# Optimization experiments

Hardware: AMD Instinct MI355X
Metric: run time of the kernel (lower is better)

Reference implementation:

```python
import jax, jax.numpy as jnp
import numpy as np
import math

B, T, C, D = 8, 2048, 1024, 1024
N_LAYER, LAYER_ID = 24, 12


def setup_inputs() -> dict:
    key = jax.random.key(0)
    ks = jax.random.split(key, 5)
    r01 = LAYER_ID / (N_LAYER - 1)
    r10 = 1.0 - LAYER_ID / N_LAYER
    ddd = np.arange(C, dtype=np.float64) / C                      # (C,)
    h = np.arange(D, dtype=np.float64)
    decay_speed = -5 + 8 * (h / (D - 1)) ** (0.7 + 1.3 * r01)     # time_decay init
    zigzag = ((np.arange(D) + 1) % 3 - 1) * 0.5
    time_first = np.log(0.3) + zigzag
    scale = C ** -0.5
    return {
        "x": jax.random.normal(ks[0], (B, T, C), jnp.float32),
        "time_decay": jnp.asarray(decay_speed, jnp.float32),
        "time_first": jnp.asarray(time_first, jnp.float32),
        "time_mix_k": jnp.asarray(ddd ** r10, jnp.float32),
        "time_mix_v": jnp.asarray(ddd ** r10 + 0.3 * r01, jnp.float32),
        "time_mix_r": jnp.asarray(ddd ** (0.5 * r10), jnp.float32),
        "Wk": jax.random.normal(ks[1], (D, C), jnp.float32) * scale,
        "Wv": jax.random.normal(ks[2], (D, C), jnp.float32) * scale,
        "Wr": jax.random.normal(ks[3], (D, C), jnp.float32) * scale,
        "Wo": jax.random.normal(ks[4], (C, D), jnp.float32) * scale,
    }


def _wkv(time_decay, time_first, k, v):
    # wkv_t = (e^{u+k_t} v_t + A_{t-1}) / (e^{u+k_t} + B_{t-1})
    # A_t = e^w A_{t-1} + e^{k_t} v_t ;  B_t likewise with v=1 ;  w = -exp(time_decay)
    # Exactly the math of the original conv1d-with-exp-curve trick, in O(T).
    ew = jnp.exp(-jnp.exp(time_decay))   # (D,)
    eu = jnp.exp(time_first)             # (D,)
    ek = jnp.exp(k)                      # [B,T,D]
    ekv = ek * v

    def step(carry, inp):
        a, b = carry                     # [B,D] each
        ekt, ekvt = inp                  # [B,D] each
        out = (eu * ekvt + a) / (eu * ekt + b)
        return (ew * a + ekvt, ew * b + ekt), out

    init = (jnp.zeros_like(ek[:, 0]), jnp.zeros_like(ek[:, 0]))
    xs = (jnp.swapaxes(ek, 0, 1), jnp.swapaxes(ekv, 0, 1))  # [T,B,D]
    _, out = jax.lax.scan(step, init, xs)
    return jnp.swapaxes(out, 0, 1)       # [B,T,D]


def reference(x, time_decay, time_first, time_mix_k, time_mix_v, time_mix_r, Wk, Wv, Wr, Wo):
    # time_shift: prepend zero row, drop last (ZeroPad2d((0,0,1,-1)))
    xx = jnp.pad(x, ((0, 0), (1, 0), (0, 0)))[:, :-1]
    xk = x * time_mix_k + xx * (1 - time_mix_k)
    xv = x * time_mix_v + xx * (1 - time_mix_v)
    xr = x * time_mix_r + xx * (1 - time_mix_r)
    k = jnp.einsum('btc,dc->btd', xk, Wk)
    v = jnp.einsum('btc,dc->btd', xv, Wv)
    sr = jax.nn.sigmoid(jnp.einsum('btc,dc->btd', xr, Wr))
    rwkv = sr * _wkv(time_decay, time_first, k, v)
    return jnp.einsum('btd,cd->btc', rwkv, Wo)
```

## Files before the change

kernel.cpp:

```cpp
#include <hip/hip_runtime.h>
#include <cstdint>
#include <cstddef>

#define Bb 8
#define Tt 2048
#define Cc 1024
#define Dd 1024
#define Mm (Bb*Tt)
#define CL 64
#define NCH (Tt/CL)


typedef __bf16  bf16x8  __attribute__((ext_vector_type(8)));
typedef float   floatx4 __attribute__((ext_vector_type(4)));

#define MFMA16(a, b, c) __builtin_amdgcn_mfma_f32_16x16x32_bf16((a), (b), (c), 0, 0, 0)

__device__ __forceinline__ ushort f2bf(float f) {
    unsigned u = __float_as_uint(f);
    u = (u + 0x7FFF + ((u >> 16) & 1)) >> 16;
    return (ushort)u;
}
__device__ __forceinline__ float bf2f(ushort u) {
    return __uint_as_float(((unsigned)u) << 16);
}

__device__ __forceinline__ void load_lds16(const void* g, void* l) {
    __builtin_amdgcn_global_load_lds((__attribute__((address_space(1))) void*)(g),
                                     (__attribute__((address_space(3))) void*)(l),
                                     16, 0, 0);
}

#define CFENCE asm volatile("" ::: "memory")
#define BARRIER do { CFENCE; __builtin_amdgcn_s_barrier(); CFENCE; } while (0)

__global__ __launch_bounds__(256) void prep_mix3(
        const float* __restrict__ x,
        const float* __restrict__ mk, const float* __restrict__ mv,
        const float* __restrict__ mr,
        ushort* __restrict__ xk, ushort* __restrict__ xv, ushort* __restrict__ xr) {
    int i  = blockIdx.x * 256 + threadIdx.x;
    int cq = i & (Cc / 8 - 1);
    int m  = i >> 7;
    int t  = m & (Tt - 1);
    float xc[8], xp[8];
    *(float4*)&xc[0] = ((const float4*)x)[i * 2];
    *(float4*)&xc[4] = ((const float4*)x)[i * 2 + 1];
    if (t != 0) {
        *(float4*)&xp[0] = ((const float4*)x)[(i - Cc / 8) * 2];
        *(float4*)&xp[4] = ((const float4*)x)[(i - Cc / 8) * 2 + 1];
    } else {
#pragma unroll
        for (int j = 0; j < 8; j++) xp[j] = 0.f;
    }
    float wk[8], wv[8], wr[8];
    *(float4*)&wk[0] = ((const float4*)mk)[cq * 2];
    *(float4*)&wk[4] = ((const float4*)mk)[cq * 2 + 1];
    *(float4*)&wv[0] = ((const float4*)mv)[cq * 2];
    *(float4*)&wv[4] = ((const float4*)mv)[cq * 2 + 1];
    *(float4*)&wr[0] = ((const float4*)mr)[cq * 2];
    *(float4*)&wr[4] = ((const float4*)mr)[cq * 2 + 1];
    ushort ok[8], ov[8], orr[8];
#pragma unroll
    for (int j = 0; j < 8; j++) {
        float d = xc[j] - xp[j];
        ok[j]  = f2bf(xp[j] + d * wk[j]);
        ov[j]  = f2bf(xp[j] + d * wv[j]);
        orr[j] = f2bf(xp[j] + d * wr[j]);
    }
    ((ulonglong2*)xk)[i] = *(const ulonglong2*)ok;
    ((ulonglong2*)xv)[i] = *(const ulonglong2*)ov;
    ((ulonglong2*)xr)[i] = *(const ulonglong2*)orr;
}

__global__ __launch_bounds__(256) void cvt_w(
        const float* __restrict__ wk, const float* __restrict__ wv,
        const float* __restrict__ wr, const float* __restrict__ wo,
        ushort* __restrict__ ok, ushort* __restrict__ ov,
        ushort* __restrict__ orr, ushort* __restrict__ oo) {
    int i = blockIdx.x * 256 + threadIdx.x;
    int sel = i >> 18;
    int j = i & ((1 << 18) - 1);
    const float* s = sel == 0 ? wk : sel == 1 ? wv : sel == 2 ? wr : wo;
    ushort* d      = sel == 0 ? ok : sel == 1 ? ov : sel == 2 ? orr : oo;
    float4 f = ((const float4*)s)[j];
    ushort4 o;
    o.x = f2bf(f.x); o.y = f2bf(f.y); o.z = f2bf(f.z); o.w = f2bf(f.w);
    ((ushort4*)d)[j] = o;
}

struct GemmR10 {
    floatx4 acc[8][4];
    int quad, fr, wm, wn;

    __device__ __forceinline__ void run(
            const ushort* __restrict__ A, const ushort* __restrict__ Bw,
            long tm, long tn, int Kdim, __bf16* LDSb) {
        const int tid  = threadIdx.x;
        const int lane = tid & 63;
        quad = lane >> 4;
        fr   = lane & 15;
        const int wave = tid >> 6;
        wm = (wave >> 2) * 128;
        wn = (wave & 3) * 64;
        const int goff = (quad ^ ((fr >> 1) & 3)) * 8;

        const int srow = tid >> 2;
        const int scol = ((tid & 3) ^ ((tid >> 3) & 3)) * 8;
        const int wlds = wave * 512;
        const ushort* Ag0 = A  + (tm + srow) * (long)Kdim + scol;
        const ushort* Ag1 = Ag0 + 128 * (long)Kdim;
        const ushort* Bg0 = Bw + (tn + srow) * (long)Kdim + scol;
        const ushort* Bg1 = Bg0 + 128 * (long)Kdim;

        auto stageA = [&](int buf, long ko) {
            __bf16* d = LDSb + buf * 16384;
            load_lds16(Ag0 + ko, d + wlds);
            load_lds16(Ag1 + ko, d + 4096 + wlds);
        };
        auto stageB = [&](int buf, long ko) {
            __bf16* d = LDSb + buf * 16384 + 8192;
            load_lds16(Bg0 + ko, d + wlds);
            load_lds16(Bg1 + ko, d + 4096 + wlds);
        };

        floatx4 zero = {0.f, 0.f, 0.f, 0.f};
#pragma unroll
        for (int ai = 0; ai < 8; ai++)
#pragma unroll
            for (int nj = 0; nj < 4; nj++) acc[ai][nj] = zero;

        const int NT = Kdim >> 5;

        stageA(0, 0);  stageB(0, 0);
        stageA(1, 32); stageB(1, 32);
        asm volatile("s_waitcnt vmcnt(4)" ::: "memory");
        BARRIER;

        int bc = 0;
        for (int T = 0; T < NT; ++T) {
            const __bf16* Ab = LDSb + bc * 16384;
            const __bf16* Bbf = Ab + 8192;
            const int sb = (bc + 2 >= 3) ? bc - 1 : bc + 2;
            const bool pf = (T + 2 < NT);
            const long ko = (long)(T + 2) * 32;

            bf16x8 a[8], b0, b1, b2, b3;
#pragma unroll
            for (int i = 0; i < 8; i++)
                a[i] = *(const bf16x8*)&Ab[(wm + i * 16 + fr) * 32 + goff];
            b0 = *(const bf16x8*)&Bbf[(wn + fr) * 32 + goff];
            b1 = *(const bf16x8*)&Bbf[(wn + 16 + fr) * 32 + goff];
            if (pf) stageA(sb, ko);
            BARRIER;
            __builtin_amdgcn_s_setprio(1);
#pragma unroll
            for (int i = 0; i < 8; i++) {
                acc[i][0] = MFMA16(a[i], b0, acc[i][0]);
                acc[i][1] = MFMA16(a[i], b1, acc[i][1]);
            }
            __builtin_amdgcn_s_setprio(0);
            BARRIER;

            b2 = *(const bf16x8*)&Bbf[(wn + 32 + fr) * 32 + goff];
            b3 = *(const bf16x8*)&Bbf[(wn + 48 + fr) * 32 + goff];
            if (pf) stageB(sb, ko);
            if (T + 1 < NT) {
                if (pf) asm volatile("s_waitcnt vmcnt(4)" ::: "memory");
                else    asm volatile("s_waitcnt vmcnt(0)" ::: "memory");
            }
            BARRIER;
            __builtin_amdgcn_s_setprio(1);
#pragma unroll
            for (int i = 0; i < 8; i++) {
                acc[i][2] = MFMA16(a[i], b2, acc[i][2]);
                acc[i][3] = MFMA16(a[i], b3, acc[i][3]);
            }
            __builtin_amdgcn_s_setprio(0);
            BARRIER;

            bc = (bc + 1 == 3) ? 0 : bc + 1;
        }
    }
};

template<int MODE>
__global__ __launch_bounds__(512, 2) void gemm_nt(
        const ushort* __restrict__ A, const ushort* __restrict__ Bw,
        void* __restrict__ Co, int Ndim, int Kdim) {
    __shared__ __attribute__((aligned(16))) __bf16 LDSb[3 * 16384];
    const int orig = blockIdx.y * 64 + blockIdx.x;
    const int L    = (orig & 7) * 32 + (orig >> 3);
    const long tm = (long)(L >> 2) * 256;
    const long tn = (long)(L & 3) * 256;
    GemmR10 g;
    g.run(A, Bw, tm, tn, Kdim, LDSb);
#pragma unroll
    for (int ai = 0; ai < 8; ai++)
#pragma unroll
        for (int nj = 0; nj < 4; nj++)
#pragma unroll
            for (int r = 0; r < 4; r++) {
                long grow = tm + g.wm + ai * 16 + g.quad * 4 + r;
                long gcol = tn + g.wn + nj * 16 + g.fr;
                float v = g.acc[ai][nj][r];
                if (MODE == 2) v = 1.f / (1.f + __expf(-v));
                if (MODE == 0)      ((float*)Co)[grow * Ndim + gcol] = v;
                else if (MODE == 3) ((_Float16*)Co)[grow * Ndim + gcol] = (_Float16)v;
                else                ((ushort*)Co)[grow * Ndim + gcol] = f2bf(v);
            }
}

__global__ __launch_bounds__(512, 2) void gemm3_nt(
        const ushort* __restrict__ xk, const ushort* __restrict__ xv,
        const ushort* __restrict__ xr,
        const ushort* __restrict__ wk, const ushort* __restrict__ wv,
        const ushort* __restrict__ wr,
        _Float16* __restrict__ kb, ushort* __restrict__ vb,
        ushort* __restrict__ sb) {
    __shared__ __attribute__((aligned(16))) __bf16 LDSb[3 * 16384];
    const int orig = blockIdx.y * 64 + blockIdx.x;
    const int L    = (orig & 7) * 96 + (orig >> 3);
    const int proj = L >> 8;
    const int rem  = L & 255;
    const long tm = (long)(rem >> 2) * 256;
    const long tn = (long)(rem & 3) * 256;
    const ushort* A  = proj == 0 ? xk : proj == 1 ? xv : xr;
    const ushort* Bw = proj == 0 ? wk : proj == 1 ? wv : wr;
    GemmR10 g;
    g.run(A, Bw, tm, tn, Cc, LDSb);
#pragma unroll
    for (int ai = 0; ai < 8; ai++)
#pragma unroll
        for (int nj = 0; nj < 4; nj++)
#pragma unroll
            for (int r = 0; r < 4; r++) {
                long grow = tm + g.wm + ai * 16 + g.quad * 4 + r;
                long gcol = tn + g.wn + nj * 16 + g.fr;
                long off = grow * Dd + gcol;
                float v = g.acc[ai][nj][r];
                if (proj == 0)      kb[off] = (_Float16)v;
                else if (proj == 1) vb[off] = f2bf(v);
                else                sb[off] = f2bf(1.f / (1.f + __expf(-v)));
            }
}

__global__ __launch_bounds__(256) void wkv_part(
        const _Float16* __restrict__ kb, const ushort* __restrict__ vb,
        const float* __restrict__ decay,
        float* __restrict__ pa, float* __restrict__ pb) {
    int gid = blockIdx.x * 256 + threadIdx.x;
    int d = gid & (Dd - 1);
    int c = (gid >> 10) & (NCH - 1);
    int b = gid >> 15;
    float ew = __expf(-__expf(decay[d]));
    size_t base = ((size_t)b * Tt + (size_t)c * CL) * Dd + d;
    float a = 0.f, bs = 0.f;
    for (int i0 = 0; i0 < CL; i0 += 8) {
        float kr[8], vr[8];
#pragma unroll
        for (int j = 0; j < 8; j++) {
            size_t idx = base + (size_t)(i0 + j) * Dd;
            kr[j] = (float)kb[idx]; vr[j] = bf2f(vb[idx]);
        }
#pragma unroll
        for (int j = 0; j < 8; j++) {
            float ek = __expf(kr[j]);
            a  = ew * a  + ek * vr[j];
            bs = ew * bs + ek;
        }
    }
    int sidx = c * (Bb * Dd) + b * Dd + d;
    pa[sidx] = a; pb[sidx] = bs;
}

__global__ __launch_bounds__(256) void wkv_prefix(
        const float* __restrict__ pa, const float* __restrict__ pb,
        const float* __restrict__ decay,
        float* __restrict__ sa, float* __restrict__ sb) {
    int gid = blockIdx.x * 256 + threadIdx.x;
    int d = gid & (Dd - 1);
    float ewL = __expf(-__expf(decay[d]) * (float)CL);
    float ca = 0.f, cb = 0.f;
#pragma unroll
    for (int c = 0; c < NCH; c++) {
        int idx = c * (Bb * Dd) + gid;
        sa[idx] = ca; sb[idx] = cb;
        ca = ewL * ca + pa[idx];
        cb = ewL * cb + pb[idx];
    }
}

__global__ __launch_bounds__(256) void wkv_chunk(
        const _Float16* __restrict__ kb, const ushort* __restrict__ vb,
        const ushort* __restrict__ sr,
        const float* __restrict__ decay, const float* __restrict__ tf,
        const float* __restrict__ sa, const float* __restrict__ sb,
        ushort* __restrict__ rw) {
    int gid = blockIdx.x * 256 + threadIdx.x;
    int d = gid & (Dd - 1);
    int c = (gid >> 10) & (NCH - 1);
    int b = gid >> 15;
    float ew = __expf(-__expf(decay[d]));
    float eu = __expf(tf[d]);
    int sidx = c * (Bb * Dd) + b * Dd + d;
    float a = sa[sidx], bs = sb[sidx];
    size_t base = ((size_t)b * Tt + (size_t)c * CL) * Dd + d;
    for (int i0 = 0; i0 < CL; i0 += 8) {
        float kr[8], vr[8], rr[8];
#pragma unroll
        for (int j = 0; j < 8; j++) {
            size_t idx = base + (size_t)(i0 + j) * Dd;
            kr[j] = (float)kb[idx]; vr[j] = bf2f(vb[idx]); rr[j] = bf2f(sr[idx]);
        }
#pragma unroll
        for (int j = 0; j < 8; j++) {
            float ek  = __expf(kr[j]);
            float ekv = ek * vr[j];
            float out = (eu * ekv + a) / (eu * ek + bs);
            a  = ew * a  + ekv;
            bs = ew * bs + ek;
            rw[base + (size_t)(i0 + j) * Dd] = f2bf(rr[j] * out);
        }
    }
}

extern "C" void kernel_launch(void* const* d_in, const int* in_sizes, int n_in,
                              void* d_out, int out_size, void* d_ws, size_t ws_size,
                              hipStream_t stream) {
    (void)in_sizes; (void)n_in; (void)out_size;
    const float* x  = (const float*)d_in[0];
    const float* td = (const float*)d_in[1];
    const float* tf = (const float*)d_in[2];
    const float* mk = (const float*)d_in[3];
    const float* mv = (const float*)d_in[4];
    const float* mr = (const float*)d_in[5];
    const float* Wk = (const float*)d_in[6];
    const float* Wv = (const float*)d_in[7];
    const float* Wr = (const float*)d_in[8];
    const float* Wo = (const float*)d_in[9];
    float* out = (float*)d_out;

    const size_t xsz = (size_t)Mm * Cc * 2;
    const size_t wsz = (size_t)Dd * Cc * 2;
    const size_t ssz = (size_t)Bb * NCH * Dd * 4;
    const size_t need_merged = 6 * xsz + 4 * wsz + 4 * ssz;

    char* p = (char*)d_ws;
    auto take = [&](size_t n) { char* r = p; p += n; return r; };
    ushort*   xk = (ushort*)take(xsz);
    ushort*   xv = (ushort*)take(xsz);
    ushort*   xr = (ushort*)take(xsz);
    _Float16* kb = (_Float16*)take(xsz);
    const bool merged = ws_size >= need_merged;
    ushort *vb, *sb, *rw;
    if (merged) {
        vb = (ushort*)take(xsz);
        sb = (ushort*)take(xsz);
        rw = xk;
    } else {
        vb = xk;
        sb = xv;
        rw = xr;
    }
    ushort* wk = (ushort*)take(wsz);
    ushort* wv = (ushort*)take(wsz);
    ushort* wr = (ushort*)take(wsz);
    ushort* wo = (ushort*)take(wsz);
    float*  pa = (float*)take(ssz);
    float*  pb = (float*)take(ssz);
    float*  sa = (float*)take(ssz);
    float*  sbst = (float*)take(ssz);

    dim3 g1(Mm / 256, Dd / 256);
    dim3 g2(Mm / 256, Cc / 256);
    dim3 g3(Mm / 256, 3 * Dd / 256);
    const int wkv_grid = (Bb * NCH * Dd) / 256;

    cvt_w<<<4096, 256, 0, stream>>>(Wk, Wv, Wr, Wo, wk, wv, wr, wo);
    prep_mix3<<<Mm * Cc / 8 / 256, 256, 0, stream>>>(x, mk, mv, mr, xk, xv, xr);

    if (merged) {
        gemm3_nt<<<g3, 512, 0, stream>>>(xk, xv, xr, wk, wv, wr, kb, vb, sb);
    } else {
        gemm_nt<3><<<g1, 512, 0, stream>>>(xk, wk, kb, Dd, Cc);
        gemm_nt<1><<<g1, 512, 0, stream>>>(xv, wv, vb, Dd, Cc);
        gemm_nt<2><<<g1, 512, 0, stream>>>(xr, wr, sb, Dd, Cc);
    }

    wkv_part  <<<wkv_grid, 256, 0, stream>>>(kb, vb, td, pa, pb);
    wkv_prefix<<<(Bb * Dd) / 256, 256, 0, stream>>>(pa, pb, td, sa, sbst);
    wkv_chunk <<<wkv_grid, 256, 0, stream>>>(kb, vb, sb, td, tf, sa, sbst, rw);

    gemm_nt<0><<<g2, 512, 0, stream>>>(rw, wo, out, Cc, Dd);
}
```

Measured before the change: 376.0 us.

## Pre-swizzle weights into MFMA fragment layout and load B directly to registers

The weight conversion kernel now writes bf16 weights in a fragment-packed layout, so the GEMM loads B operands straight from global memory into registers, double-buffered across K steps. Only A still goes through LDS, which halves LDS use and removes the B staging and one barrier pair per iteration. The WKV part and chunk kernels are also vectorised to handle 4 channels per thread with wider loads. The trade-off is that B fragments come from global/L2 without LDS reuse across waves, and fewer threads are available to hide scan latency.

```diff
diff --git a/kernel.cpp b/kernel.cpp
--- a/kernel.cpp
+++ b/kernel.cpp
@@ -13,6 +13,8 @@
 
 typedef __bf16  bf16x8  __attribute__((ext_vector_type(8)));
 typedef float   floatx4 __attribute__((ext_vector_type(4)));
+typedef _Float16 halfx4 __attribute__((ext_vector_type(4)));
+typedef unsigned short ushortx4 __attribute__((ext_vector_type(4)));
 
 #define MFMA16(a, b, c) __builtin_amdgcn_mfma_f32_16x16x32_bf16((a), (b), (c), 0, 0, 0)
 
@@ -79,22 +81,28 @@
         ushort* __restrict__ ok, ushort* __restrict__ ov,
         ushort* __restrict__ orr, ushort* __restrict__ oo) {
     int i = blockIdx.x * 256 + threadIdx.x;
-    int sel = i >> 18;
-    int j = i & ((1 << 18) - 1);
+    int fr  = i & 15;
+    int c8  = (i >> 4) & 127;
+    int nhi = (i >> 11) & 63;
+    int sel = i >> 17;
     const float* s = sel == 0 ? wk : sel == 1 ? wv : sel == 2 ? wr : wo;
     ushort* d      = sel == 0 ? ok : sel == 1 ? ov : sel == 2 ? orr : oo;
-    float4 f = ((const float4*)s)[j];
-    ushort4 o;
-    o.x = f2bf(f.x); o.y = f2bf(f.y); o.z = f2bf(f.z); o.w = f2bf(f.w);
-    ((ushort4*)d)[j] = o;
-}
-
-struct GemmR10 {
+    int n = nhi * 16 + fr;
+    const float4* src = (const float4*)(s + (size_t)n * Cc + c8 * 8);
+    float4 f0 = src[0], f1 = src[1];
+    ushort o[8];
+    o[0] = f2bf(f0.x); o[1] = f2bf(f0.y); o[2] = f2bf(f0.z); o[3] = f2bf(f0.w);
+    o[4] = f2bf(f1.x); o[5] = f2bf(f1.y); o[6] = f2bf(f1.z); o[7] = f2bf(f1.w);
+    int idx = (nhi * 32 + (c8 >> 2)) * 64 + (c8 & 3) * 16 + fr;
+    ((ulonglong2*)d)[idx] = *(const ulonglong2*)o;
+}
+
+struct GemmR11 {
     floatx4 acc[8][4];
     int quad, fr, wm, wn;
 
     __device__ __forceinline__ void run(
-            const ushort* __restrict__ A, const ushort* __restrict__ Bw,
+            const ushort* __restrict__ A, const ushort* __restrict__ Bp,
             long tm, long tn, int Kdim, __bf16* LDSb) {
         const int tid  = threadIdx.x;
         const int lane = tid & 63;
@@ -104,25 +112,21 @@
         wm = (wave >> 2) * 128;
         wn = (wave & 3) * 64;
         const int goff = (quad ^ ((fr >> 1) & 3)) * 8;
+        const int NKT  = Kdim >> 5;
 
         const int srow = tid >> 2;
         const int scol = ((tid & 3) ^ ((tid >> 3) & 3)) * 8;
         const int wlds = wave * 512;
-        const ushort* Ag0 = A  + (tm + srow) * (long)Kdim + scol;
+        const ushort* Ag0 = A + (tm + srow) * (long)Kdim + scol;
         const ushort* Ag1 = Ag0 + 128 * (long)Kdim;
-        const ushort* Bg0 = Bw + (tn + srow) * (long)Kdim + scol;
-        const ushort* Bg1 = Bg0 + 128 * (long)Kdim;
 
         auto stageA = [&](int buf, long ko) {
-            __bf16* d = LDSb + buf * 16384;
+            __bf16* d = LDSb + buf * 8192;
             load_lds16(Ag0 + ko, d + wlds);
             load_lds16(Ag1 + ko, d + 4096 + wlds);
         };
-        auto stageB = [&](int buf, long ko) {
-            __bf16* d = LDSb + buf * 16384 + 8192;
-            load_lds16(Bg0 + ko, d + wlds);
-            load_lds16(Bg1 + ko, d + 4096 + wlds);
-        };
+
+        const ushort* Bq = Bp + ((long)((tn + wn) >> 4)) * NKT * 512 + lane * 8;
 
         floatx4 zero = {0.f, 0.f, 0.f, 0.f};
 #pragma unroll
@@ -130,57 +134,57 @@
 #pragma unroll
             for (int nj = 0; nj < 4; nj++) acc[ai][nj] = zero;
 
-        const int NT = Kdim >> 5;
-
-        stageA(0, 0);  stageB(0, 0);
-        stageA(1, 32); stageB(1, 32);
-        asm volatile("s_waitcnt vmcnt(4)" ::: "memory");
+        const int NT = NKT;
+
+        stageA(0, 0);
+        stageA(1, 32);
+        bf16x8 bA[4], bB[4];
+#pragma unroll
+        for (int ni = 0; ni < 4; ni++)
+            bA[ni] = *(const bf16x8*)(Bq + (long)ni * NKT * 512);
+        asm volatile("s_waitcnt vmcnt(6)" ::: "memory");
         BARRIER;
 
-        int bc = 0;
-        for (int T = 0; T < NT; ++T) {
-            const __bf16* Ab = LDSb + bc * 16384;
-            const __bf16* Bbf = Ab + 8192;
-            const int sb = (bc + 2 >= 3) ? bc - 1 : bc + 2;
-            const bool pf = (T + 2 < NT);
-            const long ko = (long)(T + 2) * 32;
-
-            bf16x8 a[8], b0, b1, b2, b3;
-#pragma unroll
-            for (int i = 0; i < 8; i++)
-                a[i] = *(const bf16x8*)&Ab[(wm + i * 16 + fr) * 32 + goff];
-            b0 = *(const bf16x8*)&Bbf[(wn + fr) * 32 + goff];
-            b1 = *(const bf16x8*)&Bbf[(wn + 16 + fr) * 32 + goff];
-            if (pf) stageA(sb, ko);
-            BARRIER;
-            __builtin_amdgcn_s_setprio(1);
-#pragma unroll
-            for (int i = 0; i < 8; i++) {
-                acc[i][0] = MFMA16(a[i], b0, acc[i][0]);
-                acc[i][1] = MFMA16(a[i], b1, acc[i][1]);
-            }
-            __builtin_amdgcn_s_setprio(0);
-            BARRIER;
-
-            b2 = *(const bf16x8*)&Bbf[(wn + 32 + fr) * 32 + goff];
-            b3 = *(const bf16x8*)&Bbf[(wn + 48 + fr) * 32 + goff];
-            if (pf) stageB(sb, ko);
-            if (T + 1 < NT) {
-                if (pf) asm volatile("s_waitcnt vmcnt(4)" ::: "memory");
-                else    asm volatile("s_waitcnt vmcnt(0)" ::: "memory");
-            }
-            BARRIER;
-            __builtin_amdgcn_s_setprio(1);
-#pragma unroll
-            for (int i = 0; i < 8; i++) {
-                acc[i][2] = MFMA16(a[i], b2, acc[i][2]);
-                acc[i][3] = MFMA16(a[i], b3, acc[i][3]);
-            }
-            __builtin_amdgcn_s_setprio(0);
-            BARRIER;
-
-            bc = (bc + 1 == 3) ? 0 : bc + 1;
+        int slot = 0, snext = 2;
+
+#define R11_BODY(T, BC, BN)                                                   \
+        {                                                                     \
+            const __bf16* Ab = LDSb + slot * 8192;                            \
+            const bool pfB = (T) + 1 < NT;                                    \
+            const bool pfA = (T) + 2 < NT;                                    \
+            if (pfB) {                                                        \
+                _Pragma("unroll")                                             \
+                for (int ni = 0; ni < 4; ni++)                                \
+                    BN[ni] = *(const bf16x8*)(Bq + ((long)ni * NKT + (T) + 1) * 512); \
+            }                                                                 \
+            if (pfA) stageA(snext, (long)((T) + 2) * 32);                     \
+            bf16x8 a_[8];                                                     \
+            _Pragma("unroll")                                                 \
+            for (int i = 0; i < 8; i++)                                       \
+                a_[i] = *(const bf16x8*)&Ab[(wm + i * 16 + fr) * 32 + goff];  \
+            __builtin_amdgcn_s_setprio(1);                                    \
+            _Pragma("unroll")                                                 \
+            for (int i = 0; i < 8; i++) {                                     \
+                acc[i][0] = MFMA16(a_[i], BC[0], acc[i][0]);                  \
+                acc[i][1] = MFMA16(a_[i], BC[1], acc[i][1]);                  \
+                acc[i][2] = MFMA16(a_[i], BC[2], acc[i][2]);                  \
+                acc[i][3] = MFMA16(a_[i], BC[3], acc[i][3]);                  \
+            }                                                                 \
+            __builtin_amdgcn_s_setprio(0);                                    \
+            if (pfB) {                                                        \
+                if (pfA) asm volatile("s_waitcnt vmcnt(6)" ::: "memory");     \
+                else     asm volatile("s_waitcnt vmcnt(4)" ::: "memory");     \
+                BARRIER;                                                      \
+            }                                                                 \
+            slot  = (slot  + 1 == 3) ? 0 : slot  + 1;                         \
+            snext = (snext + 1 == 3) ? 0 : snext + 1;                         \
         }
+
+        for (int T = 0; T < NT; T += 2) {
+            R11_BODY(T,     bA, bB);
+            R11_BODY(T + 1, bB, bA);
+        }
+#undef R11_BODY
     }
 };
 
@@ -188,12 +192,12 @@
 __global__ __launch_bounds__(512, 2) void gemm_nt(
         const ushort* __restrict__ A, const ushort* __restrict__ Bw,
         void* __restrict__ Co, int Ndim, int Kdim) {
-    __shared__ __attribute__((aligned(16))) __bf16 LDSb[3 * 16384];
+    __shared__ __attribute__((aligned(16))) __bf16 LDSb[3 * 8192];
     const int orig = blockIdx.y * 64 + blockIdx.x;
     const int L    = (orig & 7) * 32 + (orig >> 3);
     const long tm = (long)(L >> 2) * 256;
     const long tn = (long)(L & 3) * 256;
-    GemmR10 g;
+    GemmR11 g;
     g.run(A, Bw, tm, tn, Kdim, LDSb);
 #pragma unroll
     for (int ai = 0; ai < 8; ai++)
@@ -218,7 +222,7 @@
         const ushort* __restrict__ wr,
         _Float16* __restrict__ kb, ushort* __restrict__ vb,
         ushort* __restrict__ sb) {
-    __shared__ __attribute__((aligned(16))) __bf16 LDSb[3 * 16384];
+    __shared__ __attribute__((aligned(16))) __bf16 LDSb[3 * 8192];
     const int orig = blockIdx.y * 64 + blockIdx.x;
     const int L    = (orig & 7) * 96 + (orig >> 3);
     const int proj = L >> 8;
@@ -227,7 +231,7 @@
     const long tn = (long)(rem & 3) * 256;
     const ushort* A  = proj == 0 ? xk : proj == 1 ? xv : xr;
     const ushort* Bw = proj == 0 ? wk : proj == 1 ? wv : wr;
-    GemmR10 g;
+    GemmR11 g;
     g.run(A, Bw, tm, tn, Cc, LDSb);
 #pragma unroll
     for (int ai = 0; ai < 8; ai++)
@@ -250,28 +254,28 @@
         const float* __restrict__ decay,
         float* __restrict__ pa, float* __restrict__ pb) {
     int gid = blockIdx.x * 256 + threadIdx.x;
-    int d = gid & (Dd - 1);
-    int c = (gid >> 10) & (NCH - 1);
-    int b = gid >> 15;
-    float ew = __expf(-__expf(decay[d]));
-    size_t base = ((size_t)b * Tt + (size_t)c * CL) * Dd + d;
-    float a = 0.f, bs = 0.f;
-    for (int i0 = 0; i0 < CL; i0 += 8) {
-        float kr[8], vr[8];
-#pragma unroll
-        for (int j = 0; j < 8; j++) {
-            size_t idx = base + (size_t)(i0 + j) * Dd;
-            kr[j] = (float)kb[idx]; vr[j] = bf2f(vb[idx]);
+    int d0 = (gid & 255) * 4;
+    int c  = (gid >> 8) & (NCH - 1);
+    int b  = gid >> 13;
+    float4 dec = *(const float4*)(decay + d0);
+    float ew[4] = { __expf(-__expf(dec.x)), __expf(-__expf(dec.y)),
+                    __expf(-__expf(dec.z)), __expf(-__expf(dec.w)) };
+    size_t base = ((size_t)b * Tt + (size_t)c * CL) * Dd + d0;
+    float a[4] = {0.f, 0.f, 0.f, 0.f}, bs[4] = {0.f, 0.f, 0.f, 0.f};
+    for (int t = 0; t < CL; ++t) {
+        size_t idx = base + (size_t)t * Dd;
+        halfx4   kv = *(const halfx4*)(kb + idx);
+        ushortx4 vv = *(const ushortx4*)(vb + idx);
+#pragma unroll
+        for (int j = 0; j < 4; j++) {
+            float ek = __expf((float)kv[j]);
+            a[j]  = ew[j] * a[j]  + ek * bf2f(vv[j]);
+            bs[j] = ew[j] * bs[j] + ek;
         }
-#pragma unroll
-        for (int j = 0; j < 8; j++) {
-            float ek = __expf(kr[j]);
-            a  = ew * a  + ek * vr[j];
-            bs = ew * bs + ek;
-        }
-    }
-    int sidx = c * (Bb * Dd) + b * Dd + d;
-    pa[sidx] = a; pb[sidx] = bs;
+    }
+    int sidx = c * (Bb * Dd) + b * Dd + d0;
+    *(float4*)(pa + sidx) = *(const float4*)a;
+    *(float4*)(pb + sidx) = *(const float4*)bs;
 }
 
 __global__ __launch_bounds__(256) void wkv_prefix(
@@ -298,30 +302,35 @@
         const float* __restrict__ sa, const float* __restrict__ sb,
         ushort* __restrict__ rw) {
     int gid = blockIdx.x * 256 + threadIdx.x;
-    int d = gid & (Dd - 1);
-    int c = (gid >> 10) & (NCH - 1);
-    int b = gid >> 15;
-    float ew = __expf(-__expf(decay[d]));
-    float eu = __expf(tf[d]);
-    int sidx = c * (Bb * Dd) + b * Dd + d;
-    float a = sa[sidx], bs = sb[sidx];
-    size_t base = ((size_t)b * Tt + (size_t)c * CL) * Dd + d;
-    for (int i0 = 0; i0 < CL; i0 += 8) {
-        float kr[8], vr[8], rr[8];
-#pragma unroll
-        for (int j = 0; j < 8; j++) {
-            size_t idx = base + (size_t)(i0 + j) * Dd;
-            kr[j] = (float)kb[idx]; vr[j] = bf2f(vb[idx]); rr[j] = bf2f(sr[idx]);
+    int d0 = (gid & 255) * 4;
+    int c  = (gid >> 8) & (NCH - 1);
+    int b  = gid >> 13;
+    float4 dec = *(const float4*)(decay + d0);
+    float4 tff = *(const float4*)(tf + d0);
+    float ew[4] = { __expf(-__expf(dec.x)), __expf(-__expf(dec.y)),
+                    __expf(-__expf(dec.z)), __expf(-__expf(dec.w)) };
+    float eu[4] = { __expf(tff.x), __expf(tff.y), __expf(tff.z), __expf(tff.w) };
+    int sidx = c * (Bb * Dd) + b * Dd + d0;
+    float a[4], bs[4];
+    *(float4*)a  = *(const float4*)(sa + sidx);
+    *(float4*)bs = *(const float4*)(sb + sidx);
+    size_t base = ((size_t)b * Tt + (size_t)c * CL) * Dd + d0;
+    for (int t = 0; t < CL; ++t) {
+        size_t idx = base + (size_t)t * Dd;
+        halfx4   kv = *(const halfx4*)(kb + idx);
+        ushortx4 vv = *(const ushortx4*)(vb + idx);
+        ushortx4 rv = *(const ushortx4*)(sr + idx);
+        ushortx4 ov;
+#pragma unroll
+        for (int j = 0; j < 4; j++) {
+            float ek  = __expf((float)kv[j]);
+            float ekv = ek * bf2f(vv[j]);
+            float out = (eu[j] * ekv + a[j]) / (eu[j] * ek + bs[j]);
+            a[j]  = ew[j] * a[j]  + ekv;
+            bs[j] = ew[j] * bs[j] + ek;
+            ov[j] = f2bf(bf2f(rv[j]) * out);
         }
-#pragma unroll
-        for (int j = 0; j < 8; j++) {
-            float ek  = __expf(kr[j]);
-            float ekv = ek * vr[j];
-            float out = (eu * ekv + a) / (eu * ek + bs);
-            a  = ew * a  + ekv;
-            bs = ew * bs + ek;
-            rw[base + (size_t)(i0 + j) * Dd] = f2bf(rr[j] * out);
-        }
+        *(ushortx4*)(rw + idx) = ov;
     }
 }
 
@@ -375,9 +384,9 @@
     dim3 g1(Mm / 256, Dd / 256);
     dim3 g2(Mm / 256, Cc / 256);
     dim3 g3(Mm / 256, 3 * Dd / 256);
-    const int wkv_grid = (Bb * NCH * Dd) / 256;
-
-    cvt_w<<<4096, 256, 0, stream>>>(Wk, Wv, Wr, Wo, wk, wv, wr, wo);
+    const int wkv_grid = (Bb * NCH * Dd / 4) / 256;
+
+    cvt_w<<<2048, 256, 0, stream>>>(Wk, Wv, Wr, Wo, wk, wv, wr, wo);
     prep_mix3<<<Mm * Cc / 8 / 256, 256, 0, stream>>>(x, mk, mv, mr, xk, xv, xr);
 
     if (merged) {
```

Result: slower. 408.4 us (+8.6%).
